# Optimization experiments

Measured on AMD Instinct MI355X. Metric: run time of the kernel, lower is better.

Reference implementation:

```python
import jax, jax.numpy as jnp
import numpy as np

D_MODEL = 1024
N_HEAD = 16
HEAD_DIM = D_MODEL // N_HEAD
B, S = 4, 2048


def setup_inputs() -> dict:
    key = jax.random.key(0)
    ks = jax.random.split(key, 11)
    scale = 1.0 / np.sqrt(D_MODEL)
    inp = {
        "q": jax.random.normal(ks[0], (B, S, D_MODEL), jnp.float32),
        "k": jax.random.normal(ks[1], (B, S, D_MODEL), jnp.float32),
        "v": jax.random.normal(ks[2], (B, S, D_MODEL), jnp.float32),
        # torch nn.Linear weights: [out_features, in_features], y = x @ W.T + b
        "Wq": jax.random.normal(ks[3], (D_MODEL, D_MODEL), jnp.float32) * scale,
        "bq": jax.random.normal(ks[4], (D_MODEL,), jnp.float32) * scale,
        "Wk": jax.random.normal(ks[5], (D_MODEL, D_MODEL), jnp.float32) * scale,
        "bk": jax.random.normal(ks[6], (D_MODEL,), jnp.float32) * scale,
        "Wv": jax.random.normal(ks[7], (D_MODEL, D_MODEL), jnp.float32) * scale,
        "bv": jax.random.normal(ks[8], (D_MODEL,), jnp.float32) * scale,
        "Wo": jax.random.normal(ks[9], (D_MODEL, D_MODEL), jnp.float32) * scale,
        "bo": jax.random.normal(ks[10], (D_MODEL,), jnp.float32) * scale,
    }
    return inp


def _split_heads(x):
    # [B, S, D] -> [B, H, S, hd]
    b, s, _ = x.shape
    return x.reshape(b, s, N_HEAD, HEAD_DIM).transpose(0, 2, 1, 3)


def reference(q, k, v, Wq, bq, Wk, bk, Wv, bv, Wo, bo):
    qh = _split_heads(q @ Wq.T + bq)
    kh = _split_heads(k @ Wk.T + bk)
    vh = _split_heads(v @ Wv.T + bv)
    scores = jnp.einsum("bhqd,bhkd->bhqk", qh, kh) / jnp.sqrt(
        jnp.asarray(HEAD_DIM, qh.dtype)
    )
    weights = jax.nn.softmax(scores, axis=-1)  # [B, H, Sq, Sk]
    ctx = jnp.einsum("bhqk,bhkd->bhqd", weights, vh)
    b, h, s, d = ctx.shape
    ctx = ctx.transpose(0, 2, 1, 3).reshape(b, s, h * d)  # [B, S, D]
    return ctx @ Wo.T + bo
```

## Files before the change

### kernel.cpp

```cpp
#include <hip/hip_runtime.h>
#include <hip/hip_bf16.h>

typedef float   f32x4   __attribute__((ext_vector_type(4)));
typedef __bf16  bf16x8  __attribute__((ext_vector_type(8)));
typedef unsigned short u16x8 __attribute__((ext_vector_type(8)));
typedef unsigned short u16x4 __attribute__((ext_vector_type(4)));

#define DEVI __device__ __forceinline__

DEVI unsigned short f2bf_bits(float f) {
    __bf16 h = (__bf16)f;
    return __builtin_bit_cast(unsigned short, h);
}

DEVI f32x4 mfma_bf16(bf16x8 a, bf16x8 b, f32x4 c) {
    return __builtin_amdgcn_mfma_f32_16x16x32_bf16(a, b, c, 0, 0, 0);
}

DEVI float fast_exp2(float x) {
#if __has_builtin(__builtin_amdgcn_exp2f)
    return __builtin_amdgcn_exp2f(x);
#else
    float r;
    asm("v_exp_f32 %0, %1" : "=v"(r) : "v"(x));
    return r;
#endif
}

DEVI void gload16(const void* g, void* l) {
    __builtin_amdgcn_global_load_lds(
        (const __attribute__((address_space(1))) void*)g,
        (__attribute__((address_space(3))) void*)l, 16, 0, 0);
}

__global__ __launch_bounds__(256) void convert_w_kernel(
    const float* __restrict__ Wq, const float* __restrict__ Wk,
    const float* __restrict__ Wv, unsigned short* __restrict__ Wb)
{
    int idx = blockIdx.x * 256 + threadIdx.x;
    int which = idx >> 17;
    int off = (idx & 131071) * 8;
    const float* src = which == 0 ? Wq : (which == 1 ? Wk : Wv);
    f32x4 a = *(const f32x4*)(src + off);
    f32x4 b = *(const f32x4*)(src + off + 4);
    u16x8 h;
#pragma unroll
    for (int j = 0; j < 4; ++j) { h[j] = f2bf_bits(a[j]); h[4 + j] = f2bf_bits(b[j]); }
    *(u16x8*)(Wb + (size_t)which * 1048576 + off) = h;
}

__global__ __launch_bounds__(256) void convert_wo_kernel(
    const float* __restrict__ Wo, unsigned short* __restrict__ Wb)
{
    int off = (blockIdx.x * 256 + threadIdx.x) * 8;
    f32x4 a = *(const f32x4*)(Wo + off);
    f32x4 b = *(const f32x4*)(Wo + off + 4);
    u16x8 h;
#pragma unroll
    for (int j = 0; j < 4; ++j) { h[j] = f2bf_bits(a[j]); h[4 + j] = f2bf_bits(b[j]); }
    *(u16x8*)(Wb + off) = h;
}

__global__ __launch_bounds__(256) void proj_gemm_kernel(
    const float* __restrict__ Ap, const unsigned short* __restrict__ Wb,
    const float* __restrict__ bias, unsigned short* __restrict__ Cp,
    int M, int N, int K, float scale)
{
    __shared__ __align__(16) char ldsA[128 * 128];
    __shared__ __align__(16) char ldsB[128 * 128];
    const int t = threadIdx.x;
    const int wave = t >> 6, lane = t & 63;
    const int g = lane >> 4, c = lane & 15;
    const int rowbase = blockIdx.x * 128;
    const int colbase = blockIdx.y * 128;
    const int wr = (wave >> 1) * 64, wc = (wave & 1) * 64;

    const int arow = lane >> 3;
    const int aslot = (lane & 7) ^ arow;

    const float* fbase[4];
#pragma unroll
    for (int ch = 0; ch < 4; ++ch) {
        int id = ch * 256 + t;
        int row = id >> 3;
        int col = (id & 7) * 8;
        fbase[ch] = Ap + (size_t)(rowbase + row) * K + col;
    }

    f32x4 pre0[4], pre1[4];
#pragma unroll
    for (int ch = 0; ch < 4; ++ch) {
        pre0[ch] = *(const f32x4*)(fbase[ch]);
        pre1[ch] = *(const f32x4*)(fbase[ch] + 4);
    }

    f32x4 acc[4][4] = {};

    for (int kt = 0; kt < K; kt += 64) {
#pragma unroll
        for (int j = 0; j < 4; ++j) {
            int rg = wave * 4 + j;
            int row = rg * 8 + arow;
            gload16(Wb + (size_t)(colbase + row) * K + kt + aslot * 8,
                    ldsB + rg * 1024);
        }

#pragma unroll
        for (int ch = 0; ch < 4; ++ch) {
            int id = ch * 256 + t;
            int row = id >> 3;
            int col = (id & 7) * 8;
            int dst = row * 128 + ((col * 2) ^ ((row & 7) << 4));
            u16x8 hv;
#pragma unroll
            for (int j = 0; j < 4; ++j) { hv[j] = f2bf_bits(pre0[ch][j]); hv[4 + j] = f2bf_bits(pre1[ch][j]); }
            *(u16x8*)(ldsA + dst) = hv;
        }
        __syncthreads();

        if (kt + 64 < K) {
#pragma unroll
            for (int ch = 0; ch < 4; ++ch) {
                pre0[ch] = *(const f32x4*)(fbase[ch] + kt + 64);
                pre1[ch] = *(const f32x4*)(fbase[ch] + kt + 68);
            }
        }

#pragma unroll
        for (int kk = 0; kk < 2; ++kk) {
            bf16x8 af[4], bfr[4];
#pragma unroll
            for (int i = 0; i < 4; ++i) {
                int ra = wr + i * 16 + c;
                af[i] = *(const bf16x8*)(ldsA + ra * 128 + ((kk * 64 + g * 16) ^ ((ra & 7) << 4)));
                int rb = wc + i * 16 + c;
                bfr[i] = *(const bf16x8*)(ldsB + rb * 128 + ((kk * 64 + g * 16) ^ ((rb & 7) << 4)));
            }
#pragma unroll
            for (int i = 0; i < 4; ++i)
#pragma unroll
                for (int j = 0; j < 4; ++j)
                    acc[i][j] = mfma_bf16(af[i], bfr[j], acc[i][j]);
        }
        __syncthreads();
    }

#pragma unroll
    for (int j = 0; j < 4; ++j) {
        int coln = colbase + wc + j * 16 + c;
        float bv = bias[coln];
#pragma unroll
        for (int i = 0; i < 4; ++i) {
            int row0 = rowbase + wr + i * 16 + g * 4;
#pragma unroll
            for (int r = 0; r < 4; ++r) {
                float val = (acc[i][j][r] + bv) * scale;
                Cp[(size_t)(row0 + r) * N + coln] = f2bf_bits(val);
            }
        }
    }
}

__global__ __launch_bounds__(256) void out_gemm_kernel(
    const unsigned short* __restrict__ Ab, const unsigned short* __restrict__ Wb,
    const float* __restrict__ bias, float* __restrict__ Cp,
    int M, int N, int K)
{
    __shared__ __align__(16) char ldsA[128 * 128];
    __shared__ __align__(16) char ldsB[128 * 128];
    const int t = threadIdx.x;
    const int wave = t >> 6, lane = t & 63;
    const int g = lane >> 4, c = lane & 15;
    const int rowbase = blockIdx.x * 128;
    const int colbase = blockIdx.y * 128;
    const int wr = (wave >> 1) * 64, wc = (wave & 1) * 64;

    const int arow = lane >> 3;
    const int aslot = (lane & 7) ^ arow;

    f32x4 acc[4][4] = {};

    for (int kt = 0; kt < K; kt += 64) {
#pragma unroll
        for (int j = 0; j < 4; ++j) {
            int rg = wave * 4 + j;
            int row = rg * 8 + arow;
            gload16(Ab + (size_t)(rowbase + row) * K + kt + aslot * 8,
                    ldsA + rg * 1024);
            gload16(Wb + (size_t)(colbase + row) * K + kt + aslot * 8,
                    ldsB + rg * 1024);
        }
        __syncthreads();

#pragma unroll
        for (int kk = 0; kk < 2; ++kk) {
            bf16x8 af[4], bfr[4];
#pragma unroll
            for (int i = 0; i < 4; ++i) {
                int ra = wr + i * 16 + c;
                af[i] = *(const bf16x8*)(ldsA + ra * 128 + ((kk * 64 + g * 16) ^ ((ra & 7) << 4)));
                int rb = wc + i * 16 + c;
                bfr[i] = *(const bf16x8*)(ldsB + rb * 128 + ((kk * 64 + g * 16) ^ ((rb & 7) << 4)));
            }
#pragma unroll
            for (int i = 0; i < 4; ++i)
#pragma unroll
                for (int j = 0; j < 4; ++j)
                    acc[i][j] = mfma_bf16(af[i], bfr[j], acc[i][j]);
        }
        __syncthreads();
    }

#pragma unroll
    for (int j = 0; j < 4; ++j) {
        int coln = colbase + wc + j * 16 + c;
        float bv = bias[coln];
#pragma unroll
        for (int i = 0; i < 4; ++i) {
            int row0 = rowbase + wr + i * 16 + g * 4;
#pragma unroll
            for (int r = 0; r < 4; ++r)
                Cp[(size_t)(row0 + r) * N + coln] = acc[i][j][r] + bv;
        }
    }
}

__global__ __launch_bounds__(256) void transpose_v_kernel(
    const unsigned short* __restrict__ Vp, unsigned short* __restrict__ Vt)
{
    __shared__ unsigned short tile[64][72];
    const int t = threadIdx.x;
    const int bh = blockIdx.y, b = bh >> 4, h = bh & 15;
    const int s0 = blockIdx.x * 64;
#pragma unroll
    for (int ch = 0; ch < 2; ++ch) {
        int id = ch * 256 + t;
        int srow = id >> 3, dcol = (id & 7) * 8;
        u16x8 v = *(const u16x8*)(Vp + (size_t)(b * 2048 + s0 + srow) * 1024 + h * 64 + dcol);
        *(u16x8*)&tile[srow][dcol] = v;
    }
    __syncthreads();
#pragma unroll
    for (int ch = 0; ch < 2; ++ch) {
        int id = ch * 256 + t;
        int drow = id >> 3, scol = (id & 7) * 8;
        u16x8 ov;
#pragma unroll
        for (int j = 0; j < 8; ++j) ov[j] = tile[scol + j][drow];
        *(u16x8*)(Vt + (size_t)(bh * 64 + drow) * 2048 + s0 + scol) = ov;
    }
}

__global__ __launch_bounds__(256) void attn_kernel(
    const unsigned short* __restrict__ Qp, const unsigned short* __restrict__ Kp,
    const unsigned short* __restrict__ Vt, unsigned short* __restrict__ ctx)
{
    __shared__ __align__(16) char ldsK[64 * 128];
    __shared__ __align__(16) char ldsV[64 * 128];
    __shared__ __align__(16) char ldsP[4][2][16 * 128];
    const int t = threadIdx.x;
    const int wave = t >> 6, lane = t & 63;
    const int g = lane >> 4, c = lane & 15;
    const int bh = blockIdx.y, b = bh >> 4, h = bh & 15;
    const int qb = blockIdx.x * 128;

    bf16x8 qf0[2], qf1[2];
    {
        const unsigned short* q0 = Qp + (size_t)(b * 2048 + qb + wave * 32 + c) * 1024 + h * 64;
        qf0[0] = *(const bf16x8*)(q0 + 8 * g);
        qf0[1] = *(const bf16x8*)(q0 + 32 + 8 * g);
        const unsigned short* q1 = q0 + (size_t)16 * 1024;
        qf1[0] = *(const bf16x8*)(q1 + 8 * g);
        qf1[1] = *(const bf16x8*)(q1 + 32 + 8 * g);
    }

    f32x4 o0[4] = {}, o1[4] = {};
    float psum0 = 0.f, psum1 = 0.f;

    const int row0 = t >> 3, colB = (t & 7) * 8;
    const int row1 = 32 + row0;
    const int dst0 = row0 * 128 + ((colB * 2) ^ ((row0 & 7) << 4));
    const int dst1 = row1 * 128 + ((colB * 2) ^ ((row1 & 7) << 4));
    const unsigned short* Ksrc = Kp + (size_t)(b * 2048) * 1024 + h * 64;
    const unsigned short* Vsrc = Vt + (size_t)(bh * 64) * 2048;

    u16x8 kv0 = *(const u16x8*)(Ksrc + (size_t)row0 * 1024 + colB);
    u16x8 kv1 = *(const u16x8*)(Ksrc + (size_t)row1 * 1024 + colB);
    u16x8 vv0 = *(const u16x8*)(Vsrc + (size_t)row0 * 2048 + colB);
    u16x8 vv1 = *(const u16x8*)(Vsrc + (size_t)row1 * 2048 + colB);

    char* pw0 = ldsP[wave][0];
    char* pw1 = ldsP[wave][1];

    for (int kb = 0; kb < 2048; kb += 64) {
        *(u16x8*)(ldsK + dst0) = kv0;
        *(u16x8*)(ldsK + dst1) = kv1;
        *(u16x8*)(ldsV + dst0) = vv0;
        *(u16x8*)(ldsV + dst1) = vv1;
        __syncthreads();

        if (kb + 64 < 2048) {
            kv0 = *(const u16x8*)(Ksrc + (size_t)(kb + 64 + row0) * 1024 + colB);
            kv1 = *(const u16x8*)(Ksrc + (size_t)(kb + 64 + row1) * 1024 + colB);
            vv0 = *(const u16x8*)(Vsrc + (size_t)row0 * 2048 + kb + 64 + colB);
            vv1 = *(const u16x8*)(Vsrc + (size_t)row1 * 2048 + kb + 64 + colB);
        }

        f32x4 s0[4] = {}, s1[4] = {};
#pragma unroll
        for (int kk = 0; kk < 2; ++kk) {
            bf16x8 kf[4];
#pragma unroll
            for (int ti = 0; ti < 4; ++ti) {
                int rk = ti * 16 + c;
                kf[ti] = *(const bf16x8*)(ldsK + rk * 128 + ((kk * 64 + g * 16) ^ ((rk & 7) << 4)));
            }
#pragma unroll
            for (int ti = 0; ti < 4; ++ti) {
                s0[ti] = mfma_bf16(kf[ti], qf0[kk], s0[ti]);
                s1[ti] = mfma_bf16(kf[ti], qf1[kk], s1[ti]);
            }
        }

#pragma unroll
        for (int ti = 0; ti < 4; ++ti) {
            float p0 = fast_exp2(s0[ti][0]);
            float p1 = fast_exp2(s0[ti][1]);
            float p2 = fast_exp2(s0[ti][2]);
            float p3 = fast_exp2(s0[ti][3]);
            psum0 += (p0 + p1) + (p2 + p3);
            u16x4 hp;
            hp[0] = f2bf_bits(p0); hp[1] = f2bf_bits(p1);
            hp[2] = f2bf_bits(p2); hp[3] = f2bf_bits(p3);
            *(u16x4*)(pw0 + c * 128 + ((ti * 32 + g * 8) ^ ((c & 7) << 4))) = hp;
        }
#pragma unroll
        for (int ti = 0; ti < 4; ++ti) {
            float p0 = fast_exp2(s1[ti][0]);
            float p1 = fast_exp2(s1[ti][1]);
            float p2 = fast_exp2(s1[ti][2]);
            float p3 = fast_exp2(s1[ti][3]);
            psum1 += (p0 + p1) + (p2 + p3);
            u16x4 hp;
            hp[0] = f2bf_bits(p0); hp[1] = f2bf_bits(p1);
            hp[2] = f2bf_bits(p2); hp[3] = f2bf_bits(p3);
            *(u16x4*)(pw1 + c * 128 + ((ti * 32 + g * 8) ^ ((c & 7) << 4))) = hp;
        }

#pragma unroll
        for (int kk = 0; kk < 2; ++kk) {
            bf16x8 vf[4];
#pragma unroll
            for (int ti = 0; ti < 4; ++ti) {
                int rv = ti * 16 + c;
                vf[ti] = *(const bf16x8*)(ldsV + rv * 128 + ((kk * 64 + g * 16) ^ ((rv & 7) << 4)));
            }
            bf16x8 pa0 = *(const bf16x8*)(pw0 + c * 128 + ((kk * 64 + g * 16) ^ ((c & 7) << 4)));
            bf16x8 pa1 = *(const bf16x8*)(pw1 + c * 128 + ((kk * 64 + g * 16) ^ ((c & 7) << 4)));
#pragma unroll
            for (int ti = 0; ti < 4; ++ti) {
                o0[ti] = mfma_bf16(pa0, vf[ti], o0[ti]);
                o1[ti] = mfma_bf16(pa1, vf[ti], o1[ti]);
            }
        }
        __syncthreads();
    }

    psum0 += __shfl_xor(psum0, 16);
    psum0 += __shfl_xor(psum0, 32);
    psum1 += __shfl_xor(psum1, 16);
    psum1 += __shfl_xor(psum1, 32);

#pragma unroll
    for (int r = 0; r < 4; ++r) {
        float inv0 = 1.0f / __shfl(psum0, 4 * g + r);
        float inv1 = 1.0f / __shfl(psum1, 4 * g + r);
        int row0q = qb + wave * 32 + 4 * g + r;
        int row1q = row0q + 16;
#pragma unroll
        for (int ti = 0; ti < 4; ++ti) {
            int col = h * 64 + ti * 16 + c;
            ctx[(size_t)(b * 2048 + row0q) * 1024 + col] = f2bf_bits(o0[ti][r] * inv0);
            ctx[(size_t)(b * 2048 + row1q) * 1024 + col] = f2bf_bits(o1[ti][r] * inv1);
        }
    }
}

extern "C" void kernel_launch(void* const* d_in, const int* in_sizes, int n_in,
                              void* d_out, int out_size, void* d_ws, size_t ws_size,
                              hipStream_t stream)
{
    const float* q  = (const float*)d_in[0];
    const float* k  = (const float*)d_in[1];
    const float* v  = (const float*)d_in[2];
    const float* Wq = (const float*)d_in[3];
    const float* bq = (const float*)d_in[4];
    const float* Wk = (const float*)d_in[5];
    const float* bk = (const float*)d_in[6];
    const float* Wv = (const float*)d_in[7];
    const float* bv = (const float*)d_in[8];
    const float* Wo = (const float*)d_in[9];
    const float* bo = (const float*)d_in[10];
    float* out = (float*)d_out;

    char* ws = (char*)d_ws;
    const size_t SZ = (size_t)8192 * 1024 * 2;
    unsigned short* Qp = (unsigned short*)(ws);
    unsigned short* Kp = (unsigned short*)(ws + SZ);
    unsigned short* Vp = (unsigned short*)(ws + 2 * SZ);
    unsigned short* Vt = (unsigned short*)(ws + 3 * SZ);
    unsigned short* ctx = Vp;
    unsigned short* Wbf = Vt;
    unsigned short* Wob = Kp;

    const float QSCALE = 0.1803368801111244f;

    convert_w_kernel<<<dim3(1536), 256, 0, stream>>>(Wq, Wk, Wv, Wbf);

    dim3 gg(64, 8);
    proj_gemm_kernel<<<gg, 256, 0, stream>>>(q, Wbf,           bq, Qp, 8192, 1024, 1024, QSCALE);
    proj_gemm_kernel<<<gg, 256, 0, stream>>>(k, Wbf + 1048576, bk, Kp, 8192, 1024, 1024, 1.0f);
    proj_gemm_kernel<<<gg, 256, 0, stream>>>(v, Wbf + 2097152, bv, Vp, 8192, 1024, 1024, 1.0f);
    transpose_v_kernel<<<dim3(32, 64), 256, 0, stream>>>(Vp, Vt);
    attn_kernel<<<dim3(16, 64), 256, 0, stream>>>(Qp, Kp, Vt, ctx);
    convert_wo_kernel<<<dim3(512), 256, 0, stream>>>(Wo, Wob);
    out_gemm_kernel<<<gg, 256, 0, stream>>>(ctx, Wob, bo, out, 8192, 1024, 1024);
}
```

Before: 222.1 us.

## Remap attention blocks for XCD-local K/V reuse and halve P staging LDS

The attention launch becomes a 1D grid whose block index is remapped so all query blocks of a given batch-head land on the same XCD, with the goal of sharing K/V in that die's L2 cache. The per-wave P staging buffer is cut from two 16-row tiles to one: each half's softmax probabilities are written, then consumed by the PV MFMAs, before the next half reuses the buffer. This reduces LDS use and may raise occupancy, but it serializes the two halves through LDS and reloads the V fragments twice per tile. Because each wave writes and reads only its own region, it relies on in-wave ordering of LDS accesses for correctness.

```diff
diff --git a/kernel.cpp b/kernel.cpp
--- a/kernel.cpp
+++ b/kernel.cpp
@@ -257,12 +257,17 @@
 {
     __shared__ __align__(16) char ldsK[64 * 128];
     __shared__ __align__(16) char ldsV[64 * 128];
-    __shared__ __align__(16) char ldsP[4][2][16 * 128];
+    __shared__ __align__(16) char ldsP[4][16 * 128];
     const int t = threadIdx.x;
     const int wave = t >> 6, lane = t & 63;
     const int g = lane >> 4, c = lane & 15;
-    const int bh = blockIdx.y, b = bh >> 4, h = bh & 15;
-    const int qb = blockIdx.x * 128;
+
+    const int d = blockIdx.x;
+    const int slot = d >> 3;
+    const int bh = (d & 7) * 8 + (slot >> 4);
+    const int qblk = slot & 15;
+    const int b = bh >> 4, h = bh & 15;
+    const int qb = qblk * 128;
 
     bf16x8 qf0[2], qf1[2];
     {
@@ -289,8 +294,7 @@
     u16x8 vv0 = *(const u16x8*)(Vsrc + (size_t)row0 * 2048 + colB);
     u16x8 vv1 = *(const u16x8*)(Vsrc + (size_t)row1 * 2048 + colB);
 
-    char* pw0 = ldsP[wave][0];
-    char* pw1 = ldsP[wave][1];
+    char* pw = ldsP[wave];
 
     for (int kb = 0; kb < 2048; kb += 64) {
         *(u16x8*)(ldsK + dst0) = kv0;
@@ -332,8 +336,22 @@
             u16x4 hp;
             hp[0] = f2bf_bits(p0); hp[1] = f2bf_bits(p1);
             hp[2] = f2bf_bits(p2); hp[3] = f2bf_bits(p3);
-            *(u16x4*)(pw0 + c * 128 + ((ti * 32 + g * 8) ^ ((c & 7) << 4))) = hp;
-        }
+            *(u16x4*)(pw + c * 128 + ((ti * 32 + g * 8) ^ ((c & 7) << 4))) = hp;
+        }
+#pragma unroll
+        for (int kk = 0; kk < 2; ++kk) {
+            bf16x8 vf[4];
+#pragma unroll
+            for (int ti = 0; ti < 4; ++ti) {
+                int rv = ti * 16 + c;
+                vf[ti] = *(const bf16x8*)(ldsV + rv * 128 + ((kk * 64 + g * 16) ^ ((rv & 7) << 4)));
+            }
+            bf16x8 pa = *(const bf16x8*)(pw + c * 128 + ((kk * 64 + g * 16) ^ ((c & 7) << 4)));
+#pragma unroll
+            for (int ti = 0; ti < 4; ++ti)
+                o0[ti] = mfma_bf16(pa, vf[ti], o0[ti]);
+        }
+
 #pragma unroll
         for (int ti = 0; ti < 4; ++ti) {
             float p0 = fast_exp2(s1[ti][0]);
@@ -344,9 +362,8 @@
             u16x4 hp;
             hp[0] = f2bf_bits(p0); hp[1] = f2bf_bits(p1);
             hp[2] = f2bf_bits(p2); hp[3] = f2bf_bits(p3);
-            *(u16x4*)(pw1 + c * 128 + ((ti * 32 + g * 8) ^ ((c & 7) << 4))) = hp;
-        }
-
+            *(u16x4*)(pw + c * 128 + ((ti * 32 + g * 8) ^ ((c & 7) << 4))) = hp;
+        }
 #pragma unroll
         for (int kk = 0; kk < 2; ++kk) {
             bf16x8 vf[4];
@@ -355,13 +372,10 @@
                 int rv = ti * 16 + c;
                 vf[ti] = *(const bf16x8*)(ldsV + rv * 128 + ((kk * 64 + g * 16) ^ ((rv & 7) << 4)));
             }
-            bf16x8 pa0 = *(const bf16x8*)(pw0 + c * 128 + ((kk * 64 + g * 16) ^ ((c & 7) << 4)));
-            bf16x8 pa1 = *(const bf16x8*)(pw1 + c * 128 + ((kk * 64 + g * 16) ^ ((c & 7) << 4)));
-#pragma unroll
-            for (int ti = 0; ti < 4; ++ti) {
-                o0[ti] = mfma_bf16(pa0, vf[ti], o0[ti]);
-                o1[ti] = mfma_bf16(pa1, vf[ti], o1[ti]);
-            }
+            bf16x8 pa = *(const bf16x8*)(pw + c * 128 + ((kk * 64 + g * 16) ^ ((c & 7) << 4)));
+#pragma unroll
+            for (int ti = 0; ti < 4; ++ti)
+                o1[ti] = mfma_bf16(pa, vf[ti], o1[ti]);
         }
         __syncthreads();
     }
@@ -422,7 +436,7 @@
     proj_gemm_kernel<<<gg, 256, 0, stream>>>(k, Wbf + 1048576, bk, Kp, 8192, 1024, 1024, 1.0f);
     proj_gemm_kernel<<<gg, 256, 0, stream>>>(v, Wbf + 2097152, bv, Vp, 8192, 1024, 1024, 1.0f);
     transpose_v_kernel<<<dim3(32, 64), 256, 0, stream>>>(Vp, Vt);
-    attn_kernel<<<dim3(16, 64), 256, 0, stream>>>(Qp, Kp, Vt, ctx);
+    attn_kernel<<<dim3(1024), 256, 0, stream>>>(Qp, Kp, Vt, ctx);
     convert_wo_kernel<<<dim3(512), 256, 0, stream>>>(Wo, Wob);
     out_gemm_kernel<<<gg, 256, 0, stream>>>(ctx, Wob, bo, out, 8192, 1024, 1024);
 }
```

After: 215.7 us. 2.8% less time.
